# Kernel optimization log

Hardware: AMD Instinct MI355X
Metric: run time of the kernel (lower is better)

The kernel has to match this reference:

```python
import jax, jax.numpy as jnp
import numpy as np

N = 4   # rope_mat_dim
F = 16  # num_rope_freqs


def _cayley_Q(skew_params):
    # Build skew-symmetric S: [F, N, N] from [F, N*(N-1)/2]
    iu, ju = np.triu_indices(N, 1)
    S = jnp.zeros((F, N, N), dtype=skew_params.dtype)
    S = S.at[:, iu, ju].set(skew_params)
    S = S.at[:, ju, iu].set(-skew_params)
    I = jnp.eye(N, dtype=skew_params.dtype)
    # Q = solve((I+S)^T, (I-S)^T)^T  (matches torch.linalg.solve usage)
    A = jnp.swapaxes(I + S, -1, -2)
    B = jnp.swapaxes(I - S, -1, -2)
    Q = jnp.swapaxes(jnp.linalg.solve(A, B), -1, -2)
    return Q


def setup_inputs() -> dict:
    key = jax.random.key(0)
    k1, k2 = jax.random.split(key)
    skew_params = jax.random.normal(k1, (F, N * (N - 1) // 2), dtype=jnp.float32)
    rope_matrices = jax.random.normal(k2, (4, 8192, F, N, N), dtype=jnp.float32)
    return {"skew_params": skew_params, "rope_matrices": rope_matrices}


def reference(skew_params, rope_matrices):
    Q = _cayley_Q(skew_params)                 # [F, N, N], orthogonal
    Q_inv = jnp.swapaxes(Q, -1, -2)            # Q^-1 = Q^T
    # transformed = Q @ R @ Q^-1 per (b, s, f) block
    t = jnp.einsum('fij,bsfjk->bsfik', Q, rope_matrices)
    t = jnp.einsum('bsfij,fjk->bsfik', t, Q_inv)
    return t
```

## Files before the change

kernel.cpp:

```cpp
#include <hip/hip_runtime.h>


#define NFREQ 16
#define TOTAL_BLOCKS (4 * 8192 * 16)
#define THREADS 256

__global__ __launch_bounds__(THREADS)
void rope_transform_kernel(const float* __restrict__ skew,
                           const float* __restrict__ Rin,
                           float* __restrict__ out)
{
    __shared__ float Qs[NFREQ * 17];

    const int t = threadIdx.x;
    if (t < NFREQ) {
        const double p0 = skew[t * 6 + 0];
        const double p1 = skew[t * 6 + 1];
        const double p2 = skew[t * 6 + 2];
        const double p3 = skew[t * 6 + 3];
        const double p4 = skew[t * 6 + 4];
        const double p5 = skew[t * 6 + 5];
        double M[4][4] = {
            { 1.0,  p0,  p1,  p2},
            {-p0,  1.0,  p3,  p4},
            {-p1,  -p3, 1.0,  p5},
            {-p2,  -p4, -p5, 1.0}};
        double Inv[4][4] = {{1,0,0,0},{0,1,0,0},{0,0,1,0},{0,0,0,1}};
        #pragma unroll
        for (int c = 0; c < 4; ++c) {
            const double piv = 1.0 / M[c][c];
            #pragma unroll
            for (int j = 0; j < 4; ++j) { M[c][j] *= piv; Inv[c][j] *= piv; }
            #pragma unroll
            for (int r = 0; r < 4; ++r) {
                if (r == c) continue;
                const double fac = M[r][c];
                #pragma unroll
                for (int j = 0; j < 4; ++j) {
                    M[r][j]   -= fac * M[c][j];
                    Inv[r][j] -= fac * Inv[c][j];
                }
            }
        }
        #pragma unroll
        for (int i = 0; i < 4; ++i)
            #pragma unroll
            for (int j = 0; j < 4; ++j)
                Qs[t * 17 + i * 4 + j] =
                    (float)(2.0 * Inv[i][j] - (i == j ? 1.0 : 0.0));
    }
    __syncthreads();

    const int idx = blockIdx.x * THREADS + t;
    const int f = idx & (NFREQ - 1);

    float Q[4][4];
    #pragma unroll
    for (int i = 0; i < 4; ++i)
        #pragma unroll
        for (int j = 0; j < 4; ++j)
            Q[i][j] = Qs[f * 17 + i * 4 + j];

    const float4* Rp = reinterpret_cast<const float4*>(Rin + (size_t)idx * 16);
    const float4 r0 = Rp[0], r1 = Rp[1], r2 = Rp[2], r3 = Rp[3];
    const float R[4][4] = {{r0.x, r0.y, r0.z, r0.w},
                           {r1.x, r1.y, r1.z, r1.w},
                           {r2.x, r2.y, r2.z, r2.w},
                           {r3.x, r3.y, r3.z, r3.w}};

    float T[4][4];
    #pragma unroll
    for (int i = 0; i < 4; ++i)
        #pragma unroll
        for (int k = 0; k < 4; ++k)
            T[i][k] = Q[i][0] * R[0][k] + Q[i][1] * R[1][k]
                    + Q[i][2] * R[2][k] + Q[i][3] * R[3][k];

    float4 O[4];
    #pragma unroll
    for (int i = 0; i < 4; ++i) {
        float o[4];
        #pragma unroll
        for (int k = 0; k < 4; ++k)
            o[k] = T[i][0] * Q[k][0] + T[i][1] * Q[k][1]
                 + T[i][2] * Q[k][2] + T[i][3] * Q[k][3];
        O[i] = make_float4(o[0], o[1], o[2], o[3]);
    }

    float4* Op = reinterpret_cast<float4*>(out + (size_t)idx * 16);
    Op[0] = O[0]; Op[1] = O[1]; Op[2] = O[2]; Op[3] = O[3];
}

extern "C" void kernel_launch(void* const* d_in, const int* in_sizes, int n_in,
                              void* d_out, int out_size, void* d_ws, size_t ws_size,
                              hipStream_t stream)
{
    const float* skew = (const float*)d_in[0];
    const float* Rin  = (const float*)d_in[1];
    float* out        = (float*)d_out;

    rope_transform_kernel<<<TOTAL_BLOCKS / THREADS, THREADS, 0, stream>>>(
        skew, Rin, out);
}
```

Baseline: 21.74 us.

## Split Q computation into prologue kernel and map one thread per matrix row

Moves the per-frequency Cayley inverse into a separate tiny kernel that writes Q to workspace, so each main-kernel block no longer runs serial double-precision Gaussian elimination on 16 threads before a barrier. The main kernel now assigns one thread per 4-float row instead of per 4x4 block, sharing rows among quad lanes via DPP broadcasts, so every load and store is a single coalesced float4. This adds a second kernel launch and a global round-trip for Q, and quadruples the thread count.

After: 21.18 us. -2.6%, faster.

```diff
diff --git a/kernel.cpp b/kernel.cpp
--- a/kernel.cpp
+++ b/kernel.cpp
@@ -2,93 +2,108 @@
 
 
 #define NFREQ 16
-#define TOTAL_BLOCKS (4 * 8192 * 16)
+#define NROWS (4 * 8192 * 16 * 4)
 #define THREADS 256
+#define QPAD 20
 
-__global__ __launch_bounds__(THREADS)
-void rope_transform_kernel(const float* __restrict__ skew,
-                           const float* __restrict__ Rin,
-                           float* __restrict__ out)
+__global__ void compute_Q_kernel(const float* __restrict__ skew,
+                                 float* __restrict__ Qg)
 {
-    __shared__ float Qs[NFREQ * 17];
-
     const int t = threadIdx.x;
-    if (t < NFREQ) {
-        const double p0 = skew[t * 6 + 0];
-        const double p1 = skew[t * 6 + 1];
-        const double p2 = skew[t * 6 + 2];
-        const double p3 = skew[t * 6 + 3];
-        const double p4 = skew[t * 6 + 4];
-        const double p5 = skew[t * 6 + 5];
-        double M[4][4] = {
-            { 1.0,  p0,  p1,  p2},
-            {-p0,  1.0,  p3,  p4},
-            {-p1,  -p3, 1.0,  p5},
-            {-p2,  -p4, -p5, 1.0}};
-        double Inv[4][4] = {{1,0,0,0},{0,1,0,0},{0,0,1,0},{0,0,0,1}};
+    if (t >= NFREQ) return;
+    const double p0 = skew[t * 6 + 0];
+    const double p1 = skew[t * 6 + 1];
+    const double p2 = skew[t * 6 + 2];
+    const double p3 = skew[t * 6 + 3];
+    const double p4 = skew[t * 6 + 4];
+    const double p5 = skew[t * 6 + 5];
+    double M[4][4] = {
+        { 1.0,  p0,  p1,  p2},
+        {-p0,  1.0,  p3,  p4},
+        {-p1,  -p3, 1.0,  p5},
+        {-p2,  -p4, -p5, 1.0}};
+    double Inv[4][4] = {{1,0,0,0},{0,1,0,0},{0,0,1,0},{0,0,0,1}};
+    #pragma unroll
+    for (int c = 0; c < 4; ++c) {
+        const double piv = 1.0 / M[c][c];
         #pragma unroll
-        for (int c = 0; c < 4; ++c) {
-            const double piv = 1.0 / M[c][c];
+        for (int j = 0; j < 4; ++j) { M[c][j] *= piv; Inv[c][j] *= piv; }
+        #pragma unroll
+        for (int r = 0; r < 4; ++r) {
+            if (r == c) continue;
+            const double fac = M[r][c];
             #pragma unroll
-            for (int j = 0; j < 4; ++j) { M[c][j] *= piv; Inv[c][j] *= piv; }
-            #pragma unroll
-            for (int r = 0; r < 4; ++r) {
-                if (r == c) continue;
-                const double fac = M[r][c];
-                #pragma unroll
-                for (int j = 0; j < 4; ++j) {
-                    M[r][j]   -= fac * M[c][j];
-                    Inv[r][j] -= fac * Inv[c][j];
-                }
+            for (int j = 0; j < 4; ++j) {
+                M[r][j]   -= fac * M[c][j];
+                Inv[r][j] -= fac * Inv[c][j];
             }
         }
-        #pragma unroll
-        for (int i = 0; i < 4; ++i)
-            #pragma unroll
-            for (int j = 0; j < 4; ++j)
-                Qs[t * 17 + i * 4 + j] =
-                    (float)(2.0 * Inv[i][j] - (i == j ? 1.0 : 0.0));
     }
-    __syncthreads();
-
-    const int idx = blockIdx.x * THREADS + t;
-    const int f = idx & (NFREQ - 1);
-
-    float Q[4][4];
     #pragma unroll
     for (int i = 0; i < 4; ++i)
         #pragma unroll
         for (int j = 0; j < 4; ++j)
-            Q[i][j] = Qs[f * 17 + i * 4 + j];
+            Qg[t * 16 + i * 4 + j] =
+                (float)(2.0 * Inv[i][j] - (i == j ? 1.0 : 0.0));
+}
 
-    const float4* Rp = reinterpret_cast<const float4*>(Rin + (size_t)idx * 16);
-    const float4 r0 = Rp[0], r1 = Rp[1], r2 = Rp[2], r3 = Rp[3];
-    const float R[4][4] = {{r0.x, r0.y, r0.z, r0.w},
-                           {r1.x, r1.y, r1.z, r1.w},
-                           {r2.x, r2.y, r2.z, r2.w},
-                           {r3.x, r3.y, r3.z, r3.w}};
+template <int J>
+__device__ __forceinline__ float4 quad_bcast(float4 v)
+{
+    constexpr int ctrl = J * 0x55;
+    float4 o;
+    o.x = __int_as_float(__builtin_amdgcn_mov_dpp(__float_as_int(v.x), ctrl, 0xF, 0xF, true));
+    o.y = __int_as_float(__builtin_amdgcn_mov_dpp(__float_as_int(v.y), ctrl, 0xF, 0xF, true));
+    o.z = __int_as_float(__builtin_amdgcn_mov_dpp(__float_as_int(v.z), ctrl, 0xF, 0xF, true));
+    o.w = __int_as_float(__builtin_amdgcn_mov_dpp(__float_as_int(v.w), ctrl, 0xF, 0xF, true));
+    return o;
+}
 
-    float T[4][4];
-    #pragma unroll
-    for (int i = 0; i < 4; ++i)
-        #pragma unroll
-        for (int k = 0; k < 4; ++k)
-            T[i][k] = Q[i][0] * R[0][k] + Q[i][1] * R[1][k]
-                    + Q[i][2] * R[2][k] + Q[i][3] * R[3][k];
+__device__ __forceinline__ float dot4(float4 a, float4 b)
+{
+    return a.x * b.x + a.y * b.y + a.z * b.z + a.w * b.w;
+}
 
-    float4 O[4];
-    #pragma unroll
-    for (int i = 0; i < 4; ++i) {
-        float o[4];
-        #pragma unroll
-        for (int k = 0; k < 4; ++k)
-            o[k] = T[i][0] * Q[k][0] + T[i][1] * Q[k][1]
-                 + T[i][2] * Q[k][2] + T[i][3] * Q[k][3];
-        O[i] = make_float4(o[0], o[1], o[2], o[3]);
+__global__ __launch_bounds__(THREADS)
+void rope_rows_kernel(const float* __restrict__ Qg,
+                      const float* __restrict__ Rin,
+                      float* __restrict__ out)
+{
+    __shared__ float Qs[NFREQ * QPAD];
+
+    const int t = threadIdx.x;
+    Qs[(t >> 4) * QPAD + (t & 15)] = Qg[t];
+    __syncthreads();
+
+    const int g = blockIdx.x * THREADS + t;
+    const int i = g & 3;
+    const int f = (g >> 2) & (NFREQ - 1);
+
+    const float4 r = reinterpret_cast<const float4*>(Rin)[g];
+
+    const float4* Qrow = reinterpret_cast<const float4*>(&Qs[f * QPAD]);
+    const float4 q0 = Qrow[0], q1 = Qrow[1], q2 = Qrow[2], q3 = Qrow[3];
+    const float4 qi = Qrow[i];
+
+    float4 T;
+    {
+        const float4 r0 = quad_bcast<0>(r);
+        T.x = qi.x * r0.x; T.y = qi.x * r0.y; T.z = qi.x * r0.z; T.w = qi.x * r0.w;
+        const float4 r1 = quad_bcast<1>(r);
+        T.x += qi.y * r1.x; T.y += qi.y * r1.y; T.z += qi.y * r1.z; T.w += qi.y * r1.w;
+        const float4 r2 = quad_bcast<2>(r);
+        T.x += qi.z * r2.x; T.y += qi.z * r2.y; T.z += qi.z * r2.z; T.w += qi.z * r2.w;
+        const float4 r3 = quad_bcast<3>(r);
+        T.x += qi.w * r3.x; T.y += qi.w * r3.y; T.z += qi.w * r3.z; T.w += qi.w * r3.w;
     }
 
-    float4* Op = reinterpret_cast<float4*>(out + (size_t)idx * 16);
-    Op[0] = O[0]; Op[1] = O[1]; Op[2] = O[2]; Op[3] = O[3];
+    float4 o;
+    o.x = dot4(T, q0);
+    o.y = dot4(T, q1);
+    o.z = dot4(T, q2);
+    o.w = dot4(T, q3);
+
+    reinterpret_cast<float4*>(out)[g] = o;
 }
 
 extern "C" void kernel_launch(void* const* d_in, const int* in_sizes, int n_in,
@@ -98,7 +113,8 @@
     const float* skew = (const float*)d_in[0];
     const float* Rin  = (const float*)d_in[1];
     float* out        = (float*)d_out;
+    float* Qg         = (float*)d_ws;
 
-    rope_transform_kernel<<<TOTAL_BLOCKS / THREADS, THREADS, 0, stream>>>(
-        skew, Rin, out);
+    compute_Q_kernel<<<1, 64, 0, stream>>>(skew, Qg);
+    rope_rows_kernel<<<NROWS / THREADS, THREADS, 0, stream>>>(Qg, Rin, out);
 }
```
